# Optimization experiments

Hardware: AMD Instinct MI355X
Metric: run time of the kernel (lower is better)

The kernel has to match this reference:

```python
import jax, jax.numpy as jnp
import numpy as np

N, E, IN, K, F, D = 50000, 800000, 256, 4, 64, 2


def setup_inputs() -> dict:
    key = jax.random.key(0)
    ks = jax.random.split(key, 10)
    # CSR rowptr: 0 .. E, nondecreasing, endpoints pinned
    inner = jnp.sort(jax.random.randint(ks[0], (N - 1,), 0, E + 1))
    rowptr = jnp.concatenate([jnp.zeros(1, jnp.int64), inner.astype(jnp.int64), jnp.full(1, E, jnp.int64)])
    colind = jax.random.randint(ks[1], (E,), 0, N).astype(jnp.int64)
    # CSC mirrors (used only by the fused kernel's backward; inert in forward math)
    inner_c = jnp.sort(jax.random.randint(ks[2], (N - 1,), 0, E + 1))
    colptr = jnp.concatenate([jnp.zeros(1, jnp.int64), inner_c.astype(jnp.int64), jnp.full(1, E, jnp.int64)])
    rowind = jax.random.randint(ks[3], (E,), 0, N).astype(jnp.int64)
    permute = jnp.arange(E, dtype=jnp.int64)
    feat = jax.random.normal(ks[4], (N, IN), dtype=jnp.float32)
    pseudo = jax.random.uniform(ks[5], (E, D), dtype=jnp.float32)
    # params: fc weight [K*F, IN] (xavier-normal style scale), mu ~ N(0, 0.1), inv_sigma = 1, bias = 0
    gain = float(np.sqrt(2.0))
    std = gain * float(np.sqrt(2.0 / (IN + K * F)))
    W_fc = jax.random.normal(ks[6], (K * F, IN), dtype=jnp.float32) * std
    mu = jax.random.normal(ks[7], (K, D), dtype=jnp.float32) * 0.1
    inv_sigma = jnp.ones((K, D), dtype=jnp.float32)
    bias = jnp.zeros((F,), dtype=jnp.float32)
    return {"rowptr": rowptr, "colind": colind, "colptr": colptr, "rowind": rowind,
            "permute": permute, "feat": feat, "pseudo": pseudo,
            "W_fc": W_fc, "mu": mu, "inv_sigma": inv_sigma, "bias": bias}


def reference(rowptr, colind, colptr, rowind, permute, feat, pseudo, W_fc, mu, inv_sigma, bias):
    n = feat.shape[0]
    e = colind.shape[0]
    k, d = mu.shape
    f = W_fc.shape[0] // k
    # dense projection: [N, K, F]
    node_feat = (feat @ W_fc.T).reshape(n, k, f)
    # per-edge Gaussian mixture weights: [E, K]
    diff = pseudo[:, None, :] - mu[None, :, :]              # [E, K, D]
    gaussian = jnp.exp(jnp.sum(-0.5 * diff * diff * (inv_sigma[None, :, :] ** 2), axis=-1))
    # multi-head SpMM: gather source feats, weight per kernel, sum kernels (sum commutes
    # with the segment reduction, so fold the head-sum into the edge message): [E, F]
    msg = jnp.einsum('ek,ekf->ef', gaussian, node_feat[colind])
    # destination node of each CSR edge
    dst = jnp.searchsorted(rowptr, jnp.arange(e), side='right') - 1
    rst = jax.ops.segment_sum(msg, dst, num_segments=n)      # [N, F]
    return rst + bias
```

## Files before the change

### kernel.cpp

```cpp
#include <hip/hip_runtime.h>


typedef _Float16 f16;
typedef __attribute__((ext_vector_type(4))) _Float16 f16x4;
typedef __attribute__((ext_vector_type(8))) _Float16 f16x8;
typedef __attribute__((ext_vector_type(4))) float f32x4;

__device__ inline f16x4 cvt4h(float4 v) {
    f16x4 h;
    h.x = (f16)v.x; h.y = (f16)v.y; h.z = (f16)v.z; h.w = (f16)v.w;
    return h;
}

__device__ inline int dot4_i8(int a, int b) {
#if __has_builtin(__builtin_amdgcn_sdot4)
    return __builtin_amdgcn_sdot4(a, b, 0, false);
#else
    return (int)(char)(a)       * (int)(char)(b)
         + (int)(char)(a >> 8)  * (int)(char)(b >> 8)
         + (int)(char)(a >> 16) * (int)(char)(b >> 16)
         + (int)(char)(a >> 24) * (int)(char)(b >> 24);
#endif
}

__global__ __launch_bounds__(256) void convert_W(
    const float* __restrict__ W, f16* __restrict__ Wp)
{
    const int gid = blockIdx.x * 256 + threadIdx.x;
    const int jp = gid >> 6, k4 = gid & 63;
    const int wrow = ((jp & 3) << 6) | (jp >> 2);
    reinterpret_cast<f16x4*>(Wp)[jp * 64 + k4] =
        cvt4h(reinterpret_cast<const float4*>(W)[wrow * 64 + k4]);
}

#define ASTRIDE 264
#define AS_BYTES (64 * ASTRIDE * 2)

__global__ __launch_bounds__(256) void gemm_fused(
    const float* __restrict__ feat,
    const f16* __restrict__ Wp,
    char* __restrict__ nfq,
    float* __restrict__ sc,
    int M)
{
    __shared__ char smem[AS_BYTES + 256 * 32 * 2];
    f16* As = (f16*)smem;
    f16* Bs = (f16*)(smem + AS_BYTES);
    char* qt = smem + AS_BYTES;
    const int t    = threadIdx.x;
    const int lane = t & 63;
    const int wave = t >> 6;
    const int bm   = blockIdx.x * 64;
    const int l16  = lane & 15;
    const int quad = lane >> 4;
    const int wn   = wave * 64;

    size_t bsrc[4];
#pragma unroll
    for (int j = 0; j < 4; ++j)
        bsrc[j] = (size_t)(wave * 64 + j * 16 + (lane >> 2)) * 256 + (lane & 3) * 8;

    typedef __attribute__((address_space(3))) void lds_t;
    typedef const __attribute__((address_space(1))) void gm_t;

#pragma unroll
    for (int j = 0; j < 4; ++j)
        __builtin_amdgcn_global_load_lds((gm_t*)(Wp + bsrc[j]),
            (lds_t*)(Bs + (wave * 4 + j) * 512), 16, 0, 0);

#pragma unroll
    for (int it = 0; it < 8; ++it) {
        const int flat = it * 2048 + t * 8;
        const int row  = flat >> 8;
        const int koff = flat & 255;
        const float* src = feat + (size_t)min(bm + row, M - 1) * 256 + koff;
        const float4 a0 = *reinterpret_cast<const float4*>(src);
        const float4 a1 = *reinterpret_cast<const float4*>(src + 4);
        *reinterpret_cast<f16x4*>(&As[row * ASTRIDE + koff])     = cvt4h(a0);
        *reinterpret_cast<f16x4*>(&As[row * ASTRIDE + koff + 4]) = cvt4h(a1);
    }

    f32x4 acc[4][4];
#pragma unroll
    for (int mi = 0; mi < 4; ++mi)
#pragma unroll
        for (int ni = 0; ni < 4; ++ni)
            acc[mi][ni] = (f32x4){0.f, 0.f, 0.f, 0.f};

    for (int ki = 0; ki < 8; ++ki) {
        __syncthreads();

        f16x8 af[4], bfr[4];
#pragma unroll
        for (int mi = 0; mi < 4; ++mi)
            af[mi] = *reinterpret_cast<const f16x8*>(
                &As[(mi * 16 + l16) * ASTRIDE + ki * 32 + quad * 8]);
#pragma unroll
        for (int ni = 0; ni < 4; ++ni)
            bfr[ni] = *reinterpret_cast<const f16x8*>(
                &Bs[(wn + ni * 16 + l16) * 32 + quad * 8]);

        __syncthreads();
        if (ki < 7) {
            const int k0 = (ki + 1) * 32;
#pragma unroll
            for (int j = 0; j < 4; ++j)
                __builtin_amdgcn_global_load_lds((gm_t*)(Wp + bsrc[j] + k0),
                    (lds_t*)(Bs + (wave * 4 + j) * 512), 16, 0, 0);
        }
#pragma unroll
        for (int mi = 0; mi < 4; ++mi)
#pragma unroll
            for (int ni = 0; ni < 4; ++ni)
                acc[mi][ni] = __builtin_amdgcn_mfma_f32_16x16x32_f16(
                    af[mi], bfr[ni], acc[mi][ni], 0, 0, 0);
    }

#pragma unroll
    for (int mi = 0; mi < 4; ++mi) {
#pragma unroll
        for (int r = 0; r < 4; ++r) {
            float am = 0.f;
#pragma unroll
            for (int ni = 0; ni < 4; ++ni)
                am = fmaxf(am, fabsf(acc[mi][ni][r]));
            am = fmaxf(am, __shfl_xor(am, 1));
            am = fmaxf(am, __shfl_xor(am, 2));
            am = fmaxf(am, __shfl_xor(am, 4));
            am = fmaxf(am, __shfl_xor(am, 8));
            const float sinv = am > 0.f ? 127.f / am : 0.f;
            const int rl = mi * 16 + quad * 4 + r;
#pragma unroll
            for (int ni = 0; ni < 4; ++ni)
                qt[rl * 256 + wn + ni * 16 + l16] =
                    (char)(int)__builtin_rintf(acc[mi][ni][r] * sinv);
            if (l16 == 0) {
                const int row = bm + rl;
                if (row < M) sc[row * 4 + wave] = am * (1.f / 16129.f);
            }
        }
    }
    __syncthreads();

    {
        const int rl  = t >> 2;
        const int co  = (t & 3) * 64;
        const int row = bm + rl;
        if (row < M) {
            const int4* s4 = reinterpret_cast<const int4*>(qt + rl * 256 + co);
            int4* d4 = reinterpret_cast<int4*>(nfq + (size_t)row * 256 + co);
#pragma unroll
            for (int j = 0; j < 4; ++j) d4[j] = s4[j];
        }
    }
}

__global__ __launch_bounds__(128) void edge_aggregate(
    const int* __restrict__ rowptr,
    const int* __restrict__ colind,
    const float* __restrict__ pseudo,
    const char* __restrict__ nfq,
    const float* __restrict__ sc,
    const float* __restrict__ mu,
    const float* __restrict__ inv_sigma,
    const float* __restrict__ bias,
    float* __restrict__ out,
    int N)
{
    const int wave = threadIdx.x >> 6;
    const int lane = threadIdx.x & 63;
    const int node = blockIdx.x * 2 + wave;
    if (node >= N) return;

    const int fo = lane & 15;
    const int eg = lane >> 4;
    const int qoff = fo << 4;
    const int goff = fo >> 2;

    float mxk[4], myk[4], cxk[4], cyk[4];
#pragma unroll
    for (int k = 0; k < 4; ++k) {
        mxk[k] = mu[2 * k];
        myk[k] = mu[2 * k + 1];
        const float a = inv_sigma[2 * k], b = inv_sigma[2 * k + 1];
        const float c = -0.5f * 1.4426950408889634f;
        cxk[k] = c * a * a;
        cyk[k] = c * b * b;
    }

    const int e0 = rowptr[node];
    const int e1 = rowptr[node + 1];

    float acc0 = 0.f, acc1 = 0.f, acc2 = 0.f, acc3 = 0.f;

    for (int ec = e0; ec < e1; ec += 16) {
        const int exm = ec + fo;
        const bool gv = exm < e1;
        const int ex  = gv ? exm : e1 - 1;
        const float2 p = *reinterpret_cast<const float2*>(pseudo + 2 * (size_t)ex);
        int gpk = 0;
#pragma unroll
        for (int k = 0; k < 4; ++k) {
            const float dx = p.x - mxk[k], dy = p.y - myk[k];
            const float g = exp2f(dx * dx * cxk[k] + dy * dy * cyk[k]);
            gpk |= ((int)(g * 127.f + 0.5f)) << (8 * k);
        }
        if (!gv) gpk = 0;

        int4  q[4];
        float s[4];
        int   gq[4];
#pragma unroll
        for (int gi = 0; gi < 4; ++gi) {
            const int ei = min(ec + gi * 4 + eg, e1 - 1);
            const int c  = colind[ei];
            q[gi]  = *reinterpret_cast<const int4*>(
                         nfq + ((size_t)c << 8) + qoff);
            s[gi]  = sc[c * 4 + goff];
            gq[gi] = __shfl(gpk, gi * 4 + eg);
        }
#pragma unroll
        for (int gi = 0; gi < 4; ++gi) {
            acc0 = fmaf(s[gi], (float)dot4_i8(q[gi].x, gq[gi]), acc0);
            acc1 = fmaf(s[gi], (float)dot4_i8(q[gi].y, gq[gi]), acc1);
            acc2 = fmaf(s[gi], (float)dot4_i8(q[gi].z, gq[gi]), acc2);
            acc3 = fmaf(s[gi], (float)dot4_i8(q[gi].w, gq[gi]), acc3);
        }
    }

    acc0 += __shfl_xor(acc0, 16); acc0 += __shfl_xor(acc0, 32);
    acc1 += __shfl_xor(acc1, 16); acc1 += __shfl_xor(acc1, 32);
    acc2 += __shfl_xor(acc2, 16); acc2 += __shfl_xor(acc2, 32);
    acc3 += __shfl_xor(acc3, 16); acc3 += __shfl_xor(acc3, 32);

    if (lane < 16) {
        const float4 b4 = reinterpret_cast<const float4*>(bias)[fo];
        float4 o;
        o.x = acc0 + b4.x;
        o.y = acc1 + b4.y;
        o.z = acc2 + b4.z;
        o.w = acc3 + b4.w;
        reinterpret_cast<float4*>(out + ((size_t)node << 6))[fo] = o;
    }
}

extern "C" void kernel_launch(void* const* d_in, const int* in_sizes, int n_in,
                              void* d_out, int out_size, void* d_ws, size_t ws_size,
                              hipStream_t stream)
{
    const int*   rowptr    = (const int*)d_in[0];
    const int*   colind    = (const int*)d_in[1];
    const float* feat      = (const float*)d_in[5];
    const float* pseudo    = (const float*)d_in[6];
    const float* W_fc      = (const float*)d_in[7];
    const float* mu        = (const float*)d_in[8];
    const float* inv_sigma = (const float*)d_in[9];
    const float* bias      = (const float*)d_in[10];
    float* out = (float*)d_out;

    const int N = in_sizes[0] - 1;
    char*  nfq = (char*)d_ws;
    float* sc  = (float*)(nfq + (size_t)N * 256);
    f16*   Wp  = (f16*)d_out;

    hipLaunchKernelGGL(convert_W, dim3(64), dim3(256), 0, stream, W_fc, Wp);

    hipLaunchKernelGGL(gemm_fused, dim3((N + 63) / 64), dim3(256), 0, stream,
                       feat, Wp, nfq, sc, N);

    hipLaunchKernelGGL(edge_aggregate, dim3((N + 1) / 2), dim3(128), 0, stream,
                       rowptr, colind, pseudo, nfq, sc, mu, inv_sigma, bias, out, N);
}
```

Baseline: 166.8 us.

## Process two nodes per wave and prefetch next edge chunk's colind and gaussians

Result: no change. 165.8 us (-0.6%).

```diff
diff --git a/kernel.cpp b/kernel.cpp
--- a/kernel.cpp
+++ b/kernel.cpp
@@ -155,7 +155,7 @@
     }
 }
 
-__global__ __launch_bounds__(128) void edge_aggregate(
+__global__ __launch_bounds__(256) void edge_aggregate(
     const int* __restrict__ rowptr,
     const int* __restrict__ colind,
     const float* __restrict__ pseudo,
@@ -167,13 +167,15 @@
     float* __restrict__ out,
     int N)
 {
-    const int wave = threadIdx.x >> 6;
     const int lane = threadIdx.x & 63;
-    const int node = blockIdx.x * 2 + wave;
-    if (node >= N) return;
-
-    const int fo = lane & 15;
-    const int eg = lane >> 4;
+    const int wid  = blockIdx.x * 4 + (threadIdx.x >> 6);
+    const int na   = wid * 2;
+    if (na >= N) return;
+    const int nb   = na + 1;
+    const bool hb  = nb < N;
+
+    const int fo   = lane & 15;
+    const int eg   = lane >> 4;
     const int qoff = fo << 4;
     const int goff = fo >> 2;
 
@@ -188,59 +190,120 @@
         cyk[k] = c * b * b;
     }
 
-    const int e0 = rowptr[node];
-    const int e1 = rowptr[node + 1];
-
-    float acc0 = 0.f, acc1 = 0.f, acc2 = 0.f, acc3 = 0.f;
-
-    for (int ec = e0; ec < e1; ec += 16) {
+    auto gpack = [&](int ec, int e0, int e1) -> int {
         const int exm = ec + fo;
         const bool gv = exm < e1;
-        const int ex  = gv ? exm : e1 - 1;
+        const int safe = (e1 > e0) ? (e1 - 1) : 0;
+        const int ex  = gv ? exm : safe;
         const float2 p = *reinterpret_cast<const float2*>(pseudo + 2 * (size_t)ex);
-        int gpk = 0;
+        int gp = 0;
 #pragma unroll
         for (int k = 0; k < 4; ++k) {
             const float dx = p.x - mxk[k], dy = p.y - myk[k];
-            const float g = exp2f(dx * dx * cxk[k] + dy * dy * cyk[k]);
-            gpk |= ((int)(g * 127.f + 0.5f)) << (8 * k);
-        }
-        if (!gv) gpk = 0;
-
-        int4  q[4];
-        float s[4];
-        int   gq[4];
-#pragma unroll
-        for (int gi = 0; gi < 4; ++gi) {
-            const int ei = min(ec + gi * 4 + eg, e1 - 1);
-            const int c  = colind[ei];
-            q[gi]  = *reinterpret_cast<const int4*>(
-                         nfq + ((size_t)c << 8) + qoff);
-            s[gi]  = sc[c * 4 + goff];
-            gq[gi] = __shfl(gpk, gi * 4 + eg);
-        }
-#pragma unroll
-        for (int gi = 0; gi < 4; ++gi) {
-            acc0 = fmaf(s[gi], (float)dot4_i8(q[gi].x, gq[gi]), acc0);
-            acc1 = fmaf(s[gi], (float)dot4_i8(q[gi].y, gq[gi]), acc1);
-            acc2 = fmaf(s[gi], (float)dot4_i8(q[gi].z, gq[gi]), acc2);
-            acc3 = fmaf(s[gi], (float)dot4_i8(q[gi].w, gq[gi]), acc3);
-        }
-    }
-
-    acc0 += __shfl_xor(acc0, 16); acc0 += __shfl_xor(acc0, 32);
-    acc1 += __shfl_xor(acc1, 16); acc1 += __shfl_xor(acc1, 32);
-    acc2 += __shfl_xor(acc2, 16); acc2 += __shfl_xor(acc2, 32);
-    acc3 += __shfl_xor(acc3, 16); acc3 += __shfl_xor(acc3, 32);
-
+            const float g = exp2f(fmaf(dy * dy, cyk[k], dx * dx * cxk[k]));
+            gp |= ((int)(g * 127.f + 0.5f)) << (8 * k);
+        }
+        return gv ? gp : 0;
+    };
+
+    const int ea0 = rowptr[na];
+    const int ea1 = rowptr[na + 1];
+    const int eb0 = ea1;
+    const int eb1 = hb ? rowptr[nb + 1] : ea1;
+
+    const int safea = (ea1 > ea0) ? (ea1 - 1) : 0;
+    int cfo_a = colind[min(ea0 + fo, safea)];
+    int cfo_b = 0, gpk_b = 0;
+    if (hb) {
+        const int safeb = (eb1 > eb0) ? (eb1 - 1) : 0;
+        cfo_b = colind[min(eb0 + fo, safeb)];
+        gpk_b = gpack(eb0, eb0, eb1);
+    }
+    int gpk_a = gpack(ea0, ea0, ea1);
+
+    float a0 = 0.f, a1 = 0.f, a2 = 0.f, a3 = 0.f;
+    {
+        int gpk = gpk_a, cfo = cfo_a;
+        for (int ec = ea0; ec < ea1; ec += 16) {
+            int4  q[4];
+            float s[4];
+            int   gq[4];
+#pragma unroll
+            for (int gi = 0; gi < 4; ++gi) {
+                const int c = __shfl(cfo, gi * 4 + eg);
+                q[gi]  = *reinterpret_cast<const int4*>(
+                             nfq + ((size_t)c << 8) + qoff);
+                s[gi]  = sc[c * 4 + goff];
+                gq[gi] = __shfl(gpk, gi * 4 + eg);
+            }
+            const int ecn = ec + 16;
+            int gpk_n = 0, cfo_n = cfo;
+            if (ecn < ea1) {
+                cfo_n = colind[min(ecn + fo, ea1 - 1)];
+                gpk_n = gpack(ecn, ea0, ea1);
+            }
+#pragma unroll
+            for (int gi = 0; gi < 4; ++gi) {
+                a0 = fmaf(s[gi], (float)dot4_i8(q[gi].x, gq[gi]), a0);
+                a1 = fmaf(s[gi], (float)dot4_i8(q[gi].y, gq[gi]), a1);
+                a2 = fmaf(s[gi], (float)dot4_i8(q[gi].z, gq[gi]), a2);
+                a3 = fmaf(s[gi], (float)dot4_i8(q[gi].w, gq[gi]), a3);
+            }
+            gpk = gpk_n; cfo = cfo_n;
+        }
+    }
+    a0 += __shfl_xor(a0, 16); a0 += __shfl_xor(a0, 32);
+    a1 += __shfl_xor(a1, 16); a1 += __shfl_xor(a1, 32);
+    a2 += __shfl_xor(a2, 16); a2 += __shfl_xor(a2, 32);
+    a3 += __shfl_xor(a3, 16); a3 += __shfl_xor(a3, 32);
     if (lane < 16) {
         const float4 b4 = reinterpret_cast<const float4*>(bias)[fo];
         float4 o;
-        o.x = acc0 + b4.x;
-        o.y = acc1 + b4.y;
-        o.z = acc2 + b4.z;
-        o.w = acc3 + b4.w;
-        reinterpret_cast<float4*>(out + ((size_t)node << 6))[fo] = o;
+        o.x = a0 + b4.x; o.y = a1 + b4.y; o.z = a2 + b4.z; o.w = a3 + b4.w;
+        reinterpret_cast<float4*>(out + ((size_t)na << 6))[fo] = o;
+    }
+
+    if (!hb) return;
+    float b0 = 0.f, b1 = 0.f, b2 = 0.f, b3 = 0.f;
+    {
+        int gpk = gpk_b, cfo = cfo_b;
+        for (int ec = eb0; ec < eb1; ec += 16) {
+            int4  q[4];
+            float s[4];
+            int   gq[4];
+#pragma unroll
+            for (int gi = 0; gi < 4; ++gi) {
+                const int c = __shfl(cfo, gi * 4 + eg);
+                q[gi]  = *reinterpret_cast<const int4*>(
+                             nfq + ((size_t)c << 8) + qoff);
+                s[gi]  = sc[c * 4 + goff];
+                gq[gi] = __shfl(gpk, gi * 4 + eg);
+            }
+            const int ecn = ec + 16;
+            int gpk_n = 0, cfo_n = cfo;
+            if (ecn < eb1) {
+                cfo_n = colind[min(ecn + fo, eb1 - 1)];
+                gpk_n = gpack(ecn, eb0, eb1);
+            }
+#pragma unroll
+            for (int gi = 0; gi < 4; ++gi) {
+                b0 = fmaf(s[gi], (float)dot4_i8(q[gi].x, gq[gi]), b0);
+                b1 = fmaf(s[gi], (float)dot4_i8(q[gi].y, gq[gi]), b1);
+                b2 = fmaf(s[gi], (float)dot4_i8(q[gi].z, gq[gi]), b2);
+                b3 = fmaf(s[gi], (float)dot4_i8(q[gi].w, gq[gi]), b3);
+            }
+            gpk = gpk_n; cfo = cfo_n;
+        }
+    }
+    b0 += __shfl_xor(b0, 16); b0 += __shfl_xor(b0, 32);
+    b1 += __shfl_xor(b1, 16); b1 += __shfl_xor(b1, 32);
+    b2 += __shfl_xor(b2, 16); b2 += __shfl_xor(b2, 32);
+    b3 += __shfl_xor(b3, 16); b3 += __shfl_xor(b3, 32);
+    if (lane < 16) {
+        const float4 b4 = reinterpret_cast<const float4*>(bias)[fo];
+        float4 o;
+        o.x = b0 + b4.x; o.y = b1 + b4.y; o.z = b2 + b4.z; o.w = b3 + b4.w;
+        reinterpret_cast<float4*>(out + ((size_t)nb << 6))[fo] = o;
     }
 }
 
@@ -268,6 +331,6 @@
     hipLaunchKernelGGL(gemm_fused, dim3((N + 63) / 64), dim3(256), 0, stream,
                        feat, Wp, nfq, sc, N);
 
-    hipLaunchKernelGGL(edge_aggregate, dim3((N + 1) / 2), dim3(128), 0, stream,
+    hipLaunchKernelGGL(edge_aggregate, dim3((N + 7) / 8), dim3(256), 0, stream,
                        rowptr, colind, pseudo, nfq, sc, mu, inv_sigma, bias, out, N);
 }
```
